# Kernel optimization log

Hardware: AMD Instinct MI355X
Metric: run time of the kernel (lower is better)

## Reference

```python
import jax, jax.numpy as jnp
import numpy as np

D_MODEL = 2048
NUM_HEADS = 16
HEAD_DIM = D_MODEL // NUM_HEADS


def _rotary(x, head_dim):
    # x: (..., T, head_dim). Matches torch module: half-split rotation.
    T = x.shape[-2]
    pos = jnp.arange(T, dtype=jnp.float32)[:, None]              # (T,1)
    dim = jnp.arange(head_dim // 2, dtype=jnp.float32)[None, :]  # (1,hd/2)
    angle = pos * (1.0 / jnp.power(10000.0, 2.0 * dim / head_dim))
    cos = jnp.cos(angle)  # (T, hd/2), broadcasts over leading dims
    sin = jnp.sin(angle)
    x1 = x[..., : head_dim // 2]
    x2 = x[..., head_dim // 2:]
    return jnp.concatenate([x1 * cos - x2 * sin, x2 * cos + x1 * sin], axis=-1)


def setup_inputs() -> dict:
    key = jax.random.key(0)
    ks = jax.random.split(key, 9)
    B, T, D, H, HD = 2, 2048, D_MODEL, NUM_HEADS, HEAD_DIM
    s = 1.0 / np.sqrt(D)
    return {
        "x": jax.random.normal(ks[0], (B, T, D), jnp.float32),
        "Wq": jax.random.normal(ks[1], (D, D), jnp.float32) * s,
        "bq": jnp.zeros((D,), jnp.float32),
        "Wk": jax.random.normal(ks[2], (D, HD), jnp.float32) * s,
        "bk": jnp.zeros((HD,), jnp.float32),
        "Wv": jax.random.normal(ks[3], (D, HD), jnp.float32) * s,
        "bv": jnp.zeros((HD,), jnp.float32),
        "Wo": jax.random.normal(ks[4], (D, D), jnp.float32) * s,
        "bo": jnp.zeros((D,), jnp.float32),
    }


def reference(x, Wq, bq, Wk, bk, Wv, bv, Wo, bo):
    B, T, D = x.shape
    H, HD = NUM_HEADS, HEAD_DIM
    q = (x @ Wq + bq).reshape(B, T, H, HD).transpose(0, 2, 1, 3)  # (B,H,T,hd)
    k = (x @ Wk + bk)[:, None]                                    # (B,1,T,hd)
    v = (x @ Wv + bv)[:, None]                                    # (B,1,T,hd)
    q = _rotary(q, HD)
    k = _rotary(k, HD)
    scores = jnp.einsum("bhqd,bhkd->bhqk", q, jnp.broadcast_to(k, (B, 1, T, HD))) / jnp.sqrt(jnp.float32(HD))
    attn = jax.nn.softmax(scores, axis=-1)                        # (B,H,T,T)
    ctx = jnp.einsum("bhqk,bhkd->bhqd", attn, jnp.broadcast_to(v, (B, 1, T, HD)))
    ctx = ctx.transpose(0, 2, 1, 3).reshape(B, T, D)
    return ctx @ Wo + bo
```

## Files before the change

kernel.cpp:

```cpp
#include <hip/hip_runtime.h>
#include <math.h>

#define T_SEQ  2048
#define DMODEL 2048
#define NHEADS 16
#define HDIM   128
#define MROWS  4096

typedef __attribute__((ext_vector_type(8)))  __bf16 bf16x8;
typedef __attribute__((ext_vector_type(4)))  __bf16 bf16x4;
typedef __attribute__((ext_vector_type(4)))  float  f32x4;
typedef __attribute__((ext_vector_type(16))) float  f32x16;
typedef __attribute__((ext_vector_type(4)))  unsigned int uint32x4;

#define GLOBAL_AS __attribute__((address_space(1)))
#define LDS_AS    __attribute__((address_space(3)))
__device__ __forceinline__ void async_copy16(const __bf16* g, __bf16* l) {
  __builtin_amdgcn_global_load_lds((const GLOBAL_AS void*)g, (LDS_AS void*)l, 16, 0, 0);
}

__device__ __forceinline__ unsigned int pack_bf16_2(float a, float b) {
  __bf16 x = (__bf16)a, y = (__bf16)b;
  unsigned short ux = __builtin_bit_cast(unsigned short, x);
  unsigned short uy = __builtin_bit_cast(unsigned short, y);
  return (unsigned int)ux | ((unsigned int)uy << 16);
}

__global__ __launch_bounds__(256) void prep_kernel(
    const float* __restrict__ x,
    const float* __restrict__ Wq, const float* __restrict__ Wk,
    const float* __restrict__ Wv, const float* __restrict__ Wo,
    float2* __restrict__ rope, __bf16* __restrict__ xb,
    __bf16* __restrict__ wqkvt, __bf16* __restrict__ wot)
{
  __shared__ float t[32][33];
  const int bid = blockIdx.x;
  const int tid = threadIdx.x;

  if (bid < 512) {
    int idx = bid*256 + tid;
    int d = idx & 63, pos = idx >> 6;
    double freq = pow(10000.0, -(double)d / 64.0);
    double ang = (double)pos * freq;
    rope[idx] = make_float2((float)cos(ang), (float)sin(ang));
    return;
  }
  if (bid < 512 + 8192) {
    int i = (bid - 512)*256 + tid;
    float4 v = ((const float4*)x)[i];
    bf16x4 o = { (__bf16)v.x, (__bf16)v.y, (__bf16)v.z, (__bf16)v.w };
    *(bf16x4*)(xb + (size_t)i*4) = o;
    return;
  }
  const int lb = bid - (512 + 8192);
  const int by = lb / 136;
  const int bx = lb - by*136;
  const float* src; __bf16* dst; int istride, c0, orow;
  if (bx < 64)       { src = Wq; istride = 2048; c0 = bx*32;      orow = c0;        dst = wqkvt; }
  else if (bx < 68)  { src = Wk; istride = 128;  c0 = (bx-64)*32; orow = 2048 + c0; dst = wqkvt; }
  else if (bx < 72)  { src = Wv; istride = 128;  c0 = (bx-68)*32; orow = 2176 + c0; dst = wqkvt; }
  else               { src = Wo; istride = 2048; c0 = (bx-72)*32; orow = c0;        dst = wot; }
  const int tx = tid & 31, ty = tid >> 5;
  const int r0 = by*32;
#pragma unroll
  for (int i = 0; i < 4; ++i)
    t[ty + i*8][tx] = src[(size_t)(r0 + ty + i*8)*istride + c0 + tx];
  __syncthreads();
#pragma unroll
  for (int i = 0; i < 4; ++i)
    dst[(size_t)(orow + ty + i*8)*2048 + r0 + tx] = (__bf16)t[tx][ty + i*8];
}

__global__ __launch_bounds__(256) void gemm_qkv_fused(
    const __bf16* __restrict__ A,
    const __bf16* __restrict__ Bt,
    const float* __restrict__ bq, const float* __restrict__ bk,
    const float* __restrict__ bv,
    const float2* __restrict__ rope,
    __bf16* __restrict__ qrb,
    __bf16* __restrict__ kbb,
    __bf16* __restrict__ vtb,
    float qscale)
{
  __shared__ __bf16 As[2][128*32];
  __shared__ __bf16 Bs[2][128*32];
  const int bx = blockIdx.x, by = blockIdx.y;
  const int tid = threadIdx.x;
  const int lane = tid & 63, wave = tid >> 6;
  const int quad = lane >> 4, l16 = lane & 15;
  const int m0 = (wave >> 1)*64, n0 = (wave & 1)*32;
  const int row0 = by*128, col0 = bx*128;
  const int srow = lane >> 2, scol = (lane & 3)*8;

  f32x4 acc[4][4];
#pragma unroll
  for (int i = 0; i < 4; ++i)
#pragma unroll
    for (int j = 0; j < 4; ++j) acc[i][j] = (f32x4){0.f,0.f,0.f,0.f};

  const __bf16* Ag = A  + (size_t)(row0 + wave*32 + srow)*DMODEL + scol;
  const __bf16* Bg = Bt + (size_t)(col0 + wave*32 + srow)*DMODEL + scol;
  const int woff = wave*1024;

  async_copy16(Ag,                     &As[0][woff]);
  async_copy16(Ag + (size_t)16*DMODEL, &As[0][woff + 512]);
  async_copy16(Bg,                     &Bs[0][woff]);
  async_copy16(Bg + (size_t)16*DMODEL, &Bs[0][woff + 512]);
  __syncthreads();

  int cur = 0;
  for (int kk = 0; kk < DMODEL; kk += 32) {
    if (kk + 32 < DMODEL) {
      const int nb = cur ^ 1;
      async_copy16(Ag + kk + 32,                     &As[nb][woff]);
      async_copy16(Ag + kk + 32 + (size_t)16*DMODEL, &As[nb][woff + 512]);
      async_copy16(Bg + kk + 32,                     &Bs[nb][woff]);
      async_copy16(Bg + kk + 32 + (size_t)16*DMODEL, &Bs[nb][woff + 512]);
    }
    bf16x8 af[4], bfr[4];
#pragma unroll
    for (int i = 0; i < 4; ++i)
      af[i] = *(const bf16x8*)&As[cur][(m0 + i*16 + l16)*32 + quad*8];
#pragma unroll
    for (int j = 0; j < 4; ++j) {
      const int cb = n0 + (j & 1)*16 + (j >> 1)*64;
      bfr[j] = *(const bf16x8*)&Bs[cur][(cb + l16)*32 + quad*8];
    }
#pragma unroll
    for (int i = 0; i < 4; ++i)
#pragma unroll
      for (int j = 0; j < 4; ++j)
        acc[i][j] = __builtin_amdgcn_mfma_f32_16x16x32_bf16(af[i], bfr[j], acc[i][j], 0,0,0);
    __syncthreads();
    cur ^= 1;
  }

  if (bx == 17) {
#pragma unroll
    for (int j = 0; j < 2; ++j) {
      const int d = n0 + j*16 + l16;
      const float b1 = bv[d], b2 = bv[d + 64];
#pragma unroll
      for (int i = 0; i < 4; ++i) {
        const int rg = row0 + m0 + i*16 + quad*4;
        const int bb = rg >> 11, t0 = rg & (T_SEQ-1);
        bf16x4 p1, p2;
#pragma unroll
        for (int r = 0; r < 4; ++r) {
          p1[r] = (__bf16)(acc[i][j][r]   + b1);
          p2[r] = (__bf16)(acc[i][j+2][r] + b2);
        }
        *(bf16x4*)&vtb[((size_t)bb*128 + d)*T_SEQ + t0]      = p1;
        *(bf16x4*)&vtb[((size_t)bb*128 + d + 64)*T_SEQ + t0] = p2;
      }
    }
    return;
  }

  const float* bias_p; float scale; __bf16* obase; int ostride;
  if (bx < 16)      { bias_p = bq + bx*128; scale = qscale;
                      obase = qrb + bx*128; ostride = 2048; }
  else              { bias_p = bk; scale = 1.f;
                      obase = kbb; ostride = 128; }

#pragma unroll
  for (int j = 0; j < 2; ++j) {
    const int d = n0 + j*16 + l16;
    const float b1 = bias_p[d], b2 = bias_p[d + 64];
#pragma unroll
    for (int i = 0; i < 4; ++i) {
      const int rl = m0 + i*16 + quad*4;
#pragma unroll
      for (int r = 0; r < 4; ++r) {
        const int rg = row0 + rl + r;
        const float x1 = acc[i][j][r]   + b1;
        const float x2 = acc[i][j+2][r] + b2;
        float2 cs = rope[(size_t)(rg & (T_SEQ-1))*64 + d];
        obase[(size_t)rg*ostride + d]      = (__bf16)((x1*cs.x - x2*cs.y)*scale);
        obase[(size_t)rg*ostride + d + 64] = (__bf16)((x2*cs.x + x1*cs.y)*scale);
      }
    }
  }
}

__global__ __launch_bounds__(256) void gemm_bf16_t128(
    const __bf16* __restrict__ A, const __bf16* __restrict__ Bt,
    const float* __restrict__ bias, float* __restrict__ C,
    int M, int N, int K)
{
  __shared__ __bf16 As[2][128*32];
  __shared__ __bf16 Bs[2][128*32];
  const int tid = threadIdx.x;
  const int lane = tid & 63, wave = tid >> 6;
  const int quad = lane >> 4, l16 = lane & 15;
  const int m0 = (wave & 1)*64, n0 = (wave >> 1)*64;
  const int row0 = blockIdx.y*128, col0 = blockIdx.x*128;
  const int srow = lane >> 2, scol = (lane & 3)*8;

  f32x4 acc[4][4];
#pragma unroll
  for (int i = 0; i < 4; ++i)
#pragma unroll
    for (int j = 0; j < 4; ++j) acc[i][j] = (f32x4){0.f,0.f,0.f,0.f};

  const __bf16* Ag = A  + (size_t)(row0 + wave*32 + srow)*K + scol;
  const __bf16* Bg = Bt + (size_t)(col0 + wave*32 + srow)*K + scol;
  const int woff = wave*1024;

  async_copy16(Ag,                &As[0][woff]);
  async_copy16(Ag + (size_t)16*K, &As[0][woff + 512]);
  async_copy16(Bg,                &Bs[0][woff]);
  async_copy16(Bg + (size_t)16*K, &Bs[0][woff + 512]);
  __syncthreads();

  int cur = 0;
  for (int kk = 0; kk < K; kk += 32) {
    if (kk + 32 < K) {
      const int nb = cur ^ 1;
      async_copy16(Ag + kk + 32,                &As[nb][woff]);
      async_copy16(Ag + kk + 32 + (size_t)16*K, &As[nb][woff + 512]);
      async_copy16(Bg + kk + 32,                &Bs[nb][woff]);
      async_copy16(Bg + kk + 32 + (size_t)16*K, &Bs[nb][woff + 512]);
    }
    bf16x8 af[4], bfr[4];
#pragma unroll
    for (int i = 0; i < 4; ++i)
      af[i] = *(const bf16x8*)&As[cur][(m0 + i*16 + l16)*32 + quad*8];
#pragma unroll
    for (int j = 0; j < 4; ++j)
      bfr[j] = *(const bf16x8*)&Bs[cur][(n0 + j*16 + l16)*32 + quad*8];
#pragma unroll
    for (int i = 0; i < 4; ++i)
#pragma unroll
      for (int j = 0; j < 4; ++j)
        acc[i][j] = __builtin_amdgcn_mfma_f32_16x16x32_bf16(af[i], bfr[j], acc[i][j], 0,0,0);
    __syncthreads();
    cur ^= 1;
  }
#pragma unroll
  for (int j = 0; j < 4; ++j) {
    const int ccol = col0 + n0 + j*16 + l16;
    const float bvv = bias[ccol];
#pragma unroll
    for (int i = 0; i < 4; ++i) {
      const int crow = row0 + m0 + i*16 + quad*4;
#pragma unroll
      for (int r = 0; r < 4; ++r)
        C[(size_t)(crow + r)*N + ccol] = acc[i][j][r] + bvv;
    }
  }
}

#define KSTR 136
#define VSTR 72
__global__ __launch_bounds__(256) void mqa_attn_mfma(
    const __bf16* __restrict__ qb,
    const __bf16* __restrict__ kb,
    const __bf16* __restrict__ vt,
    __bf16* __restrict__ ctx)
{
  __shared__ __bf16 Ks[64*KSTR];
  __shared__ __bf16 Vs[128*VSTR];
  __shared__ float  Linv[128];
  const int tid = threadIdx.x, lane = tid & 63, wave = tid >> 6;
  const int h5 = lane >> 5, l32 = lane & 31;
  const int h = blockIdx.y, b = blockIdx.z;
  const int qbase = blockIdx.x*128 + wave*32;

  bf16x8 qf[8];
  const __bf16* qp = qb + ((size_t)b*T_SEQ + qbase + l32)*DMODEL + h*HDIM;
#pragma unroll
  for (int ds = 0; ds < 8; ++ds) qf[ds] = *(const bf16x8*)(qp + ds*16 + h5*8);

  f32x16 oacc[4];
#pragma unroll
  for (int g = 0; g < 4; ++g)
#pragma unroll
    for (int r = 0; r < 16; ++r) oacc[g][r] = 0.f;
  float lsum = 0.f;

  const __bf16* kbase = kb + (size_t)b*T_SEQ*HDIM;
  const __bf16* vbase = vt + (size_t)b*HDIM*T_SEQ;

  for (int kt = 0; kt < T_SEQ/64; ++kt) {
    __syncthreads();
#pragma unroll
    for (int i = 0; i < 4; ++i) {
      int idx = i*256 + tid;
      int key = idx >> 4, c = idx & 15;
      *(bf16x8*)&Ks[key*KSTR + c*8] =
          *(const bf16x8*)(kbase + (size_t)(kt*64 + key)*HDIM + c*8);
    }
#pragma unroll
    for (int i = 0; i < 4; ++i) {
      int idx = i*256 + tid;
      int d = idx >> 3, c = idx & 7;
      *(bf16x8*)&Vs[d*VSTR + c*8] =
          *(const bf16x8*)(vbase + (size_t)d*T_SEQ + kt*64 + c*8);
    }
    __syncthreads();

    f32x16 sacc[2];
#pragma unroll
    for (int kg = 0; kg < 2; ++kg) {
#pragma unroll
      for (int r = 0; r < 16; ++r) sacc[kg][r] = 0.f;
      __builtin_amdgcn_s_setprio(1);
#pragma unroll
      for (int ds = 0; ds < 8; ++ds) {
        bf16x8 kf = *(const bf16x8*)&Ks[(kg*32 + l32)*KSTR + ds*16 + h5*8];
        sacc[kg] = __builtin_amdgcn_mfma_f32_32x32x16_bf16(kf, qf[ds], sacc[kg], 0,0,0);
      }
      __builtin_amdgcn_s_setprio(0);
    }

    bf16x8 pf[4];
#pragma unroll
    for (int kg = 0; kg < 2; ++kg) {
      unsigned int w[8];
#pragma unroll
      for (int m = 0; m < 8; ++m) {
        float p0 = __builtin_amdgcn_exp2f(sacc[kg][2*m]);
        float p1 = __builtin_amdgcn_exp2f(sacc[kg][2*m+1]);
        lsum += p0; lsum += p1;
        w[m] = pack_bf16_2(p0, p1);
      }
#pragma unroll
      for (int kss = 0; kss < 2; ++kss) {
        auto s1 = __builtin_amdgcn_permlane32_swap(w[4*kss+0], w[4*kss+2], false, false);
        auto s2 = __builtin_amdgcn_permlane32_swap(w[4*kss+1], w[4*kss+3], false, false);
        uint32x4 u = (uint32x4){ s1[0], s2[0], s1[1], s2[1] };
        pf[kg*2 + kss] = __builtin_bit_cast(bf16x8, u);
      }
    }

    __builtin_amdgcn_s_setprio(1);
#pragma unroll
    for (int ks = 0; ks < 4; ++ks) {
#pragma unroll
      for (int g = 0; g < 4; ++g) {
        bf16x8 vf = *(const bf16x8*)&Vs[(g*32 + l32)*VSTR + ks*16 + h5*8];
        oacc[g] = __builtin_amdgcn_mfma_f32_32x32x16_bf16(pf[ks], vf, oacc[g], 0,0,0);
      }
    }
    __builtin_amdgcn_s_setprio(0);
  }

  lsum += __shfl_xor(lsum, 32);
  if (h5 == 0) Linv[wave*32 + l32] = 1.f / lsum;
  __asm__ volatile("s_waitcnt lgkmcnt(0)" ::: "memory");

  __bf16* op = ctx + ((size_t)b*T_SEQ + qbase)*DMODEL + h*HDIM + l32;
#pragma unroll
  for (int r1 = 0; r1 < 4; ++r1) {
    float4 iv = *(const float4*)&Linv[wave*32 + r1*8 + h5*4];
#pragma unroll
    for (int r0 = 0; r0 < 4; ++r0) {
      int qrow = r1*8 + h5*4 + r0;
#pragma unroll
      for (int g = 0; g < 4; ++g)
        op[(size_t)qrow*DMODEL + g*32] = (__bf16)(oacc[g][r1*4 + r0] * (&iv.x)[r0]);
    }
  }
}

extern "C" void kernel_launch(void* const* d_in, const int* in_sizes, int n_in,
                              void* d_out, int out_size, void* d_ws, size_t ws_size,
                              hipStream_t stream) {
  const float* x  = (const float*)d_in[0];
  const float* Wq = (const float*)d_in[1];
  const float* bq = (const float*)d_in[2];
  const float* Wk = (const float*)d_in[3];
  const float* bk = (const float*)d_in[4];
  const float* Wv = (const float*)d_in[5];
  const float* bv = (const float*)d_in[6];
  const float* Wo = (const float*)d_in[7];
  const float* bo = (const float*)d_in[8];
  float* out = (float*)d_out;

  uint8_t* ws = (uint8_t*)d_ws;
  __bf16* qrb  = (__bf16*)(ws);
  __bf16* xb   = (__bf16*)(ws + 16777216);
  __bf16* wqkvt= (__bf16*)(ws + 33554432);
  __bf16* wot  = (__bf16*)(ws + 42991616);
  __bf16* kbb  = (__bf16*)(ws + 51380224);
  __bf16* vtb  = (__bf16*)(ws + 53477376);
  float2* rope = (float2*)(ws + 54525952);

  const float qscale = 1.4426950408889634f * 0.08838834764831845f;

  prep_kernel<<<dim3(17408), 256, 0, stream>>>(x, Wq, Wk, Wv, Wo, rope, xb, wqkvt, wot);

  gemm_qkv_fused<<<dim3(18,32), 256, 0, stream>>>(
      xb, wqkvt, bq, bk, bv, rope, qrb, kbb, vtb, qscale);

  mqa_attn_mfma<<<dim3(16,16,2), 256, 0, stream>>>(qrb, kbb, vtb, xb);

  gemm_bf16_t128<<<dim3(16,32), 256, 0, stream>>>(xb, wot, bo, out, MROWS, DMODEL, DMODEL);
}
```

Baseline: 334.3 us.

## Single-buffer QKV GEMM and use partial vmcnt waits in output GEMM

The fused QKV GEMM drops its LDS double buffer and now loads each k-tile synchronously, with barriers before and after the copy. This halves its shared-memory footprint, which may allow more blocks per CU, but the global loads no longer overlap the MFMA work. The output GEMM keeps double buffering but replaces __syncthreads with an explicit s_waitcnt vmcnt(4) plus raw s_barrier and sched_barriers. That lets the prefetch of the next tile stay in flight while the current tile is consumed, and peels the last iteration out of the loop. The hand-written waitcnt counts on the compiler emitting exactly four loads per iteration, so the ordering is fragile if codegen changes.

```diff
diff --git a/kernel.cpp b/kernel.cpp
--- a/kernel.cpp
+++ b/kernel.cpp
@@ -82,8 +82,8 @@
     __bf16* __restrict__ vtb,
     float qscale)
 {
-  __shared__ __bf16 As[2][128*32];
-  __shared__ __bf16 Bs[2][128*32];
+  __shared__ __bf16 As[128*32];
+  __shared__ __bf16 Bs[128*32];
   const int bx = blockIdx.x, by = blockIdx.y;
   const int tid = threadIdx.x;
   const int lane = tid & 63, wave = tid >> 6;
@@ -100,39 +100,30 @@
 
   const __bf16* Ag = A  + (size_t)(row0 + wave*32 + srow)*DMODEL + scol;
   const __bf16* Bg = Bt + (size_t)(col0 + wave*32 + srow)*DMODEL + scol;
-  const int woff = wave*1024;
-
-  async_copy16(Ag,                     &As[0][woff]);
-  async_copy16(Ag + (size_t)16*DMODEL, &As[0][woff + 512]);
-  async_copy16(Bg,                     &Bs[0][woff]);
-  async_copy16(Bg + (size_t)16*DMODEL, &Bs[0][woff + 512]);
-  __syncthreads();
-
-  int cur = 0;
+  __bf16* AsW = &As[wave*1024];
+  __bf16* BsW = &Bs[wave*1024];
+
   for (int kk = 0; kk < DMODEL; kk += 32) {
-    if (kk + 32 < DMODEL) {
-      const int nb = cur ^ 1;
-      async_copy16(Ag + kk + 32,                     &As[nb][woff]);
-      async_copy16(Ag + kk + 32 + (size_t)16*DMODEL, &As[nb][woff + 512]);
-      async_copy16(Bg + kk + 32,                     &Bs[nb][woff]);
-      async_copy16(Bg + kk + 32 + (size_t)16*DMODEL, &Bs[nb][woff + 512]);
-    }
+    __syncthreads();
+    async_copy16(Ag + kk,                     AsW);
+    async_copy16(Ag + kk + (size_t)16*DMODEL, AsW + 512);
+    async_copy16(Bg + kk,                     BsW);
+    async_copy16(Bg + kk + (size_t)16*DMODEL, BsW + 512);
+    __syncthreads();
     bf16x8 af[4], bfr[4];
 #pragma unroll
     for (int i = 0; i < 4; ++i)
-      af[i] = *(const bf16x8*)&As[cur][(m0 + i*16 + l16)*32 + quad*8];
+      af[i] = *(const bf16x8*)&As[(m0 + i*16 + l16)*32 + quad*8];
 #pragma unroll
     for (int j = 0; j < 4; ++j) {
       const int cb = n0 + (j & 1)*16 + (j >> 1)*64;
-      bfr[j] = *(const bf16x8*)&Bs[cur][(cb + l16)*32 + quad*8];
+      bfr[j] = *(const bf16x8*)&Bs[(cb + l16)*32 + quad*8];
     }
 #pragma unroll
     for (int i = 0; i < 4; ++i)
 #pragma unroll
       for (int j = 0; j < 4; ++j)
         acc[i][j] = __builtin_amdgcn_mfma_f32_16x16x32_bf16(af[i], bfr[j], acc[i][j], 0,0,0);
-    __syncthreads();
-    cur ^= 1;
   }
 
   if (bx == 17) {
@@ -211,17 +202,41 @@
   async_copy16(Ag + (size_t)16*K, &As[0][woff + 512]);
   async_copy16(Bg,                &Bs[0][woff]);
   async_copy16(Bg + (size_t)16*K, &Bs[0][woff + 512]);
-  __syncthreads();
 
   int cur = 0;
-  for (int kk = 0; kk < K; kk += 32) {
-    if (kk + 32 < K) {
-      const int nb = cur ^ 1;
-      async_copy16(Ag + kk + 32,                &As[nb][woff]);
-      async_copy16(Ag + kk + 32 + (size_t)16*K, &As[nb][woff + 512]);
-      async_copy16(Bg + kk + 32,                &Bs[nb][woff]);
-      async_copy16(Bg + kk + 32 + (size_t)16*K, &Bs[nb][woff + 512]);
-    }
+  for (int kk = 0; kk < K - 32; kk += 32) {
+    const int nb = cur ^ 1;
+    async_copy16(Ag + kk + 32,                &As[nb][woff]);
+    async_copy16(Ag + kk + 32 + (size_t)16*K, &As[nb][woff + 512]);
+    async_copy16(Bg + kk + 32,                &Bs[nb][woff]);
+    async_copy16(Bg + kk + 32 + (size_t)16*K, &Bs[nb][woff + 512]);
+    asm volatile("s_waitcnt vmcnt(4)" ::: "memory");
+    __builtin_amdgcn_sched_barrier(0);
+    __builtin_amdgcn_s_barrier();
+    __builtin_amdgcn_sched_barrier(0);
+    {
+      bf16x8 af[4], bfr[4];
+#pragma unroll
+      for (int i = 0; i < 4; ++i)
+        af[i] = *(const bf16x8*)&As[cur][(m0 + i*16 + l16)*32 + quad*8];
+#pragma unroll
+      for (int j = 0; j < 4; ++j)
+        bfr[j] = *(const bf16x8*)&Bs[cur][(n0 + j*16 + l16)*32 + quad*8];
+#pragma unroll
+      for (int i = 0; i < 4; ++i)
+#pragma unroll
+        for (int j = 0; j < 4; ++j)
+          acc[i][j] = __builtin_amdgcn_mfma_f32_16x16x32_bf16(af[i], bfr[j], acc[i][j], 0,0,0);
+    }
+    __builtin_amdgcn_sched_barrier(0);
+    __builtin_amdgcn_s_barrier();
+    cur = nb;
+  }
+  asm volatile("s_waitcnt vmcnt(0)" ::: "memory");
+  __builtin_amdgcn_sched_barrier(0);
+  __builtin_amdgcn_s_barrier();
+  __builtin_amdgcn_sched_barrier(0);
+  {
     bf16x8 af[4], bfr[4];
 #pragma unroll
     for (int i = 0; i < 4; ++i)
@@ -234,9 +249,8 @@
 #pragma unroll
       for (int j = 0; j < 4; ++j)
         acc[i][j] = __builtin_amdgcn_mfma_f32_16x16x32_bf16(af[i], bfr[j], acc[i][j], 0,0,0);
-    __syncthreads();
-    cur ^= 1;
-  }
+  }
+
 #pragma unroll
   for (int j = 0; j < 4; ++j) {
     const int ccol = col0 + n0 + j*16 + l16;
```

Measured after the change: 326.2 us. 1.02x faster.
